# Kernel optimization log

Hardware: AMD Instinct MI355X
Metric: run time of the kernel (lower is better)

Reference implementation:

```python
import jax, jax.numpy as jnp
import numpy as np

N_NODES = 50000
N_EDGES = 800000
FIN = 128
FQK = 128
FV = 128
H = 8


def setup_inputs() -> dict:
    key = jax.random.key(0)
    k1, k2, k3, k4, k5 = jax.random.split(key, 5)
    x = jax.random.normal(k1, (N_NODES, FIN), dtype=jnp.float32)
    # nn.Linear(Fin, 2*Fqk+Fv, bias=False): weight shape [Ftot, Fin]
    W = jax.random.normal(k2, (2 * FQK + FV, FIN), dtype=jnp.float32) / np.sqrt(FIN)
    # src must be sorted (scatter_* assume batch[-1]+1 segments)
    src = jnp.sort(jax.random.randint(k3, (N_EDGES,), 0, N_NODES))
    dest = jax.random.randint(k4, (N_EDGES,), 0, N_NODES)
    ei = jnp.stack([src, dest])
    batch = jnp.sort(jax.random.randint(k5, (N_NODES,), 0, 64))
    return {"x": x, "W": W, "batch": batch, "ei": ei}


def reference(x, W, batch, ei):
    n = x.shape[0]
    Fh = FQK // H    # 16
    Fhv = FV // H    # 16
    scaling = float(Fh) ** (-0.5)
    src, dest = ei[0], ei[1]

    qkv = x @ W.T                                   # [n, 2*Fqk+Fv]
    q = (qkv[:, :FQK] * scaling).reshape(n, H, Fh)
    k = qkv[:, FQK:2 * FQK].reshape(n, H, Fh)
    v = qkv[:, 2 * FQK:].reshape(n, H, Fhv)

    # per-edge attention scores, one per head: [E, H]
    aw = jnp.einsum('ehf,ehf->eh', q[src], k[dest])
    # faithful to original scatter_softmax: subtract GLOBAL per-head max
    aw = aw - aw.max(axis=0)
    ex = jnp.exp(aw)
    denom = jax.ops.segment_sum(ex, src, num_segments=n)[src]   # [E, H]
    a = ex / denom

    out = jax.ops.segment_sum(a[:, :, None] * v[dest], src, num_segments=n)  # [n, H, Fhv]
    return out.reshape(n, H * Fhv)
```

## Files before the change

kernel.cpp:

```cpp
#include <hip/hip_runtime.h>
#include <hip/hip_fp16.h>
#include <math.h>

#define FIN_ 128
#define NGB_ 3

typedef _Float16 half2v __attribute__((ext_vector_type(2)));
typedef _Float16 half8v __attribute__((ext_vector_type(8)));
typedef __attribute__((ext_vector_type(4))) float float4v;

__device__ __forceinline__ half2v u2h(unsigned u) {
    union { unsigned u; half2v h; } c; c.u = u; return c.h;
}

__device__ __forceinline__ half8v cvt8(float4 a, float4 b) {
    half8v r;
    r[0] = (_Float16)a.x; r[1] = (_Float16)a.y;
    r[2] = (_Float16)a.z; r[3] = (_Float16)a.w;
    r[4] = (_Float16)b.x; r[5] = (_Float16)b.y;
    r[6] = (_Float16)b.z; r[7] = (_Float16)b.w;
    return r;
}

__global__ __launch_bounds__(256) void prep_kernel(const float* __restrict__ x,
                                                   const float* __restrict__ W,
                                                   _Float16* __restrict__ qb,
                                                   _Float16* __restrict__ kv,
                                                   const int* __restrict__ src,
                                                   int* __restrict__ rowptr,
                                                   int n, int nE, int nxb) {
    const int bid = blockIdx.x;
    const int t = threadIdx.x;

    if (bid >= 3 * nxb) {
        const int i = (bid - 3 * nxb) * 256 + t;
        if (i > n) return;
        int lo = 0, hi = nE;
        while (lo < hi) {
            int mid = (lo + hi) >> 1;
            if (src[mid] < i) lo = mid + 1; else hi = mid;
        }
        rowptr[i] = lo;
        return;
    }

    __shared__ _Float16 T[64][136];
    const int bx = bid / 3, fsel = bid % 3;
    const int row0 = bx * 128;
    const int f0 = fsel * 128;
    const int lane = t & 63;
    const int wave = t >> 6;
    const int wr = wave >> 1, wc = wave & 1;
    const int l15 = lane & 15, kg = lane >> 4;

    float4v acc[4][4];
#pragma unroll
    for (int i = 0; i < 4; ++i)
#pragma unroll
        for (int j = 0; j < 4; ++j) acc[i][j] = (float4v)0.f;

    int nodeIdx[4];
#pragma unroll
    for (int ni = 0; ni < 4; ++ni) {
        const int nd = row0 + wc * 64 + ni * 16 + l15;
        nodeIdx[ni] = (nd < n) ? nd : 0;
    }
    const size_t fbase = (size_t)(f0 + wr * 64 + l15) * FIN_;

#pragma unroll
    for (int half = 0; half < 2; ++half) {
#pragma unroll
        for (int ks = 0; ks < 2; ++ks) {
            const int koff = half * 64 + ks * 32 + kg * 8;
            half8v a[4], b[4];
#pragma unroll
            for (int mi = 0; mi < 4; ++mi) {
                const float* p = W + fbase + (size_t)mi * 16 * FIN_ + koff;
                a[mi] = cvt8(*(const float4*)p, *(const float4*)(p + 4));
            }
#pragma unroll
            for (int ni = 0; ni < 4; ++ni) {
                const float* p = x + (size_t)nodeIdx[ni] * FIN_ + koff;
                b[ni] = cvt8(*(const float4*)p, *(const float4*)(p + 4));
            }
#pragma unroll
            for (int mi = 0; mi < 4; ++mi)
#pragma unroll
                for (int ni = 0; ni < 4; ++ni)
                    acc[mi][ni] = __builtin_amdgcn_mfma_f32_16x16x32_f16(
                        a[mi], b[ni], acc[mi][ni], 0, 0, 0);
        }
    }

    const bool isq = (fsel == 0);
    const float s = isq ? 0.25f : 1.0f;
    for (int ph = 0; ph < 2; ++ph) {
        if (wc == ph) {
#pragma unroll
            for (int mi = 0; mi < 4; ++mi) {
                const int fb = wr * 64 + mi * 16 + kg * 4;
#pragma unroll
                for (int ni = 0; ni < 4; ++ni) {
                    const int nl = ni * 16 + l15;
                    union { ushort4 u; _Float16 f[4]; } pk;
#pragma unroll
                    for (int r = 0; r < 4; ++r) pk.f[r] = (_Float16)(acc[mi][ni][r] * s);
                    *(ushort4*)&T[nl][fb] = pk.u;
                }
            }
        }
        __syncthreads();
#pragma unroll
        for (int i = 0; i < 4; ++i) {
            const int u = t + i * 256;
            const int nl = u >> 4;
            const int cs = (u & 15) * 8;
            const int ng = row0 + ph * 64 + nl;
            if (ng < n) {
                const half8v val = *(const half8v*)&T[nl][cs];
                if (isq) *(half8v*)&qb[(size_t)ng * 128 + cs] = val;
                else     *(half8v*)&kv[(size_t)ng * 256 + (f0 - 128) + cs] = val;
            }
        }
        __syncthreads();
    }
}

__device__ __forceinline__ float dot16(uint4 k0, uint4 k1, const half2v* q) {
#if __has_builtin(__builtin_amdgcn_fdot2)
    float s = __builtin_amdgcn_fdot2(u2h(k0.x), q[0], 0.f, false);
    s = __builtin_amdgcn_fdot2(u2h(k0.y), q[1], s, false);
    s = __builtin_amdgcn_fdot2(u2h(k0.z), q[2], s, false);
    s = __builtin_amdgcn_fdot2(u2h(k0.w), q[3], s, false);
    s = __builtin_amdgcn_fdot2(u2h(k1.x), q[4], s, false);
    s = __builtin_amdgcn_fdot2(u2h(k1.y), q[5], s, false);
    s = __builtin_amdgcn_fdot2(u2h(k1.z), q[6], s, false);
    s = __builtin_amdgcn_fdot2(u2h(k1.w), q[7], s, false);
    return s;
#else
    half2v a = u2h(k0.x) * q[0];
    a += u2h(k0.y) * q[1];
    a += u2h(k0.z) * q[2];
    a += u2h(k0.w) * q[3];
    a += u2h(k1.x) * q[4];
    a += u2h(k1.y) * q[5];
    a += u2h(k1.z) * q[6];
    a += u2h(k1.w) * q[7];
    return (float)a[0] + (float)a[1];
#endif
}

__global__ __launch_bounds__(256) void attn_edges_ep(const _Float16* __restrict__ qb,
                                                     const _Float16* __restrict__ kv,
                                                     const int* __restrict__ rowptr,
                                                     const int* __restrict__ dest,
                                                     float* __restrict__ out, int n) {
    const int wave = threadIdx.x >> 6;
    const int node = blockIdx.x * 4 + wave;
    if (node >= n) return;
    const int lane = threadIdx.x & 63;
    const int j = lane >> 3;
    const int h = lane & 7;
    const int ppos = ((j & 1) << 3) | ((j & 2) << 1) | ((j & 4) >> 1);
    float* outp = &out[(size_t)node * FIN_ + h * 16 + ppos];

    const int e0 = rowptr[node];
    const int e1 = rowptr[node + 1];
    if (e0 == e1) {
        *(float2*)outp = make_float2(0.f, 0.f);
        return;
    }

    half2v qh[8];
    {
        const uint4 q0 = *(const uint4*)(qb + (size_t)node * 128 + h * 16);
        const uint4 q1 = *(const uint4*)(qb + (size_t)node * 128 + h * 16 + 8);
        qh[0] = u2h(q0.x); qh[1] = u2h(q0.y); qh[2] = u2h(q0.z); qh[3] = u2h(q0.w);
        qh[4] = u2h(q1.x); qh[5] = u2h(q1.y); qh[6] = u2h(q1.z); qh[7] = u2h(q1.w);
    }

    float lsum = 0.f;
    half2v a8[8];
#pragma unroll
    for (int i = 0; i < 8; ++i) a8[i] = (half2v)(_Float16)0;

    const int hoff = h << 4;
    for (int eb = e0; eb < e1; eb += 16) {
        const int eA = eb + j;
        const int eB = eb + 8 + j;
        const bool vA = eA < e1;
        const bool vB = eB < e1;
        const unsigned dA = (unsigned)dest[vA ? eA : (e1 - 1)];
        const unsigned dB = (unsigned)dest[vB ? eB : (e1 - 1)];
        const unsigned offA = (dA << 8) + hoff;
        const unsigned offB = (dB << 8) + hoff;
        const uint4 k0A = *(const uint4*)(kv + offA);
        const uint4 k1A = *(const uint4*)(kv + offA + 8);
        const uint4 v0A = *(const uint4*)(kv + offA + 128);
        const uint4 v1A = *(const uint4*)(kv + offA + 136);
        const uint4 k0B = *(const uint4*)(kv + offB);
        const uint4 k1B = *(const uint4*)(kv + offB + 8);
        const uint4 v0B = *(const uint4*)(kv + offB + 128);
        const uint4 v1B = *(const uint4*)(kv + offB + 136);

        const float sA = dot16(k0A, k1A, qh);
        const float sB = dot16(k0B, k1B, qh);
        const float pA = vA ? __expf(sA) : 0.f;
        const float pB = vB ? __expf(sB) : 0.f;
        lsum += pA + pB;

        const _Float16 ha = (_Float16)pA, hb = (_Float16)pB;
        const half2v pa = {ha, ha}, pb = {hb, hb};
        a8[0] += pa * u2h(v0A.x) + pb * u2h(v0B.x);
        a8[1] += pa * u2h(v0A.y) + pb * u2h(v0B.y);
        a8[2] += pa * u2h(v0A.z) + pb * u2h(v0B.z);
        a8[3] += pa * u2h(v0A.w) + pb * u2h(v0B.w);
        a8[4] += pa * u2h(v1A.x) + pb * u2h(v1B.x);
        a8[5] += pa * u2h(v1A.y) + pb * u2h(v1B.y);
        a8[6] += pa * u2h(v1A.z) + pb * u2h(v1B.z);
        a8[7] += pa * u2h(v1A.w) + pb * u2h(v1B.w);
    }

    lsum += __shfl_xor(lsum, 8);
    lsum += __shfl_xor(lsum, 16);
    lsum += __shfl_xor(lsum, 32);

    float a16[16];
#pragma unroll
    for (int i = 0; i < 8; ++i) {
        a16[2 * i]     = (float)a8[i][0];
        a16[2 * i + 1] = (float)a8[i][1];
    }

    float r8[8];
    {
        const bool b = (j & 1) != 0;
#pragma unroll
        for (int i = 0; i < 8; ++i) {
            const float keep = b ? a16[i + 8] : a16[i];
            const float send = b ? a16[i] : a16[i + 8];
            r8[i] = keep + __shfl_xor(send, 8);
        }
    }
    float r4[4];
    {
        const bool b = (j & 2) != 0;
#pragma unroll
        for (int i = 0; i < 4; ++i) {
            const float keep = b ? r8[i + 4] : r8[i];
            const float send = b ? r8[i] : r8[i + 4];
            r4[i] = keep + __shfl_xor(send, 16);
        }
    }
    float r2[2];
    {
        const bool b = (j & 4) != 0;
#pragma unroll
        for (int i = 0; i < 2; ++i) {
            const float keep = b ? r4[i + 2] : r4[i];
            const float send = b ? r4[i] : r4[i + 2];
            r2[i] = keep + __shfl_xor(send, 32);
        }
    }

    const float inv = (lsum > 0.f) ? 1.f / lsum : 0.f;
    *(float2*)outp = make_float2(r2[0] * inv, r2[1] * inv);
}

extern "C" void kernel_launch(void* const* d_in, const int* in_sizes, int n_in,
                              void* d_out, int out_size, void* d_ws, size_t ws_size,
                              hipStream_t stream) {
    const float* x = (const float*)d_in[0];
    const float* W = (const float*)d_in[1];
    const int* ei = (const int*)d_in[3];

    const int n = in_sizes[0] / FIN_;
    const int nE = in_sizes[3] / 2;
    const int* src = ei;
    const int* dest = ei + nE;

    char* w = (char*)d_ws;
    _Float16* qb = (_Float16*)w;   w += (size_t)n * 128 * 2;
    _Float16* kv = (_Float16*)w;   w += (size_t)n * 256 * 2;
    int* rowptr = (int*)w;
    float* out = (float*)d_out;

    const int nxb = (n + 127) / 128;
    const int nrb = (n + 1 + 255) / 256;
    prep_kernel<<<3 * nxb + nrb, 256, 0, stream>>>(x, W, qb, kv, src, rowptr, n, nE, nxb);

    attn_edges_ep<<<(n + 3) / 4, 256, 0, stream>>>(qb, kv, rowptr, dest, out, n);
}
```

Measured before the change: 104.9 us.

## Retile QKV projection to 32-node blocks computing all 384 features per block

The GEMM part of the prep kernel now gives each block 32 nodes and all three Q/K/V feature groups, in place of 128 nodes by one 128-feature group. Each x row is therefore read once rather than three times, and there are many more, smaller blocks, which improves occupancy and load balance on a GPU with many compute units. The rowptr binary-search blocks move to the front of the grid so they get scheduled early. The trade-off is that W is re-read by every block, though at 384x128 it should stay in cache, and the MFMA tile per wave is smaller, with 12 accumulators per wave rather than 16.

```diff
diff --git a/kernel.cpp b/kernel.cpp
--- a/kernel.cpp
+++ b/kernel.cpp
@@ -3,7 +3,6 @@
 #include <math.h>
 
 #define FIN_ 128
-#define NGB_ 3
 
 typedef _Float16 half2v __attribute__((ext_vector_type(2)));
 typedef _Float16 half8v __attribute__((ext_vector_type(8)));
@@ -28,12 +27,12 @@
                                                    _Float16* __restrict__ kv,
                                                    const int* __restrict__ src,
                                                    int* __restrict__ rowptr,
-                                                   int n, int nE, int nxb) {
+                                                   int n, int nE, int nrb) {
     const int bid = blockIdx.x;
     const int t = threadIdx.x;
 
-    if (bid >= 3 * nxb) {
-        const int i = (bid - 3 * nxb) * 256 + t;
+    if (bid < nrb) {
+        const int i = bid * 256 + t;
         if (i > n) return;
         int lo = 0, hi = nE;
         while (lo < hi) {
@@ -44,82 +43,71 @@
         return;
     }
 
-    __shared__ _Float16 T[64][136];
-    const int bx = bid / 3, fsel = bid % 3;
-    const int row0 = bx * 128;
-    const int f0 = fsel * 128;
+    __shared__ _Float16 T[32][136];
+    const int row0 = (bid - nrb) * 32;
     const int lane = t & 63;
-    const int wave = t >> 6;
-    const int wr = wave >> 1, wc = wave & 1;
+    const int wv = t >> 6;
     const int l15 = lane & 15, kg = lane >> 4;
 
-    float4v acc[4][4];
-#pragma unroll
-    for (int i = 0; i < 4; ++i)
-#pragma unroll
-        for (int j = 0; j < 4; ++j) acc[i][j] = (float4v)0.f;
-
-    int nodeIdx[4];
-#pragma unroll
-    for (int ni = 0; ni < 4; ++ni) {
-        const int nd = row0 + wc * 64 + ni * 16 + l15;
+    float4v acc[6][2];
+#pragma unroll
+    for (int g = 0; g < 6; ++g)
+#pragma unroll
+        for (int j = 0; j < 2; ++j) acc[g][j] = (float4v)0.f;
+
+    int nodeIdx[2];
+#pragma unroll
+    for (int ni = 0; ni < 2; ++ni) {
+        const int nd = row0 + ni * 16 + l15;
         nodeIdx[ni] = (nd < n) ? nd : 0;
     }
-    const size_t fbase = (size_t)(f0 + wr * 64 + l15) * FIN_;
-
-#pragma unroll
-    for (int half = 0; half < 2; ++half) {
-#pragma unroll
-        for (int ks = 0; ks < 2; ++ks) {
-            const int koff = half * 64 + ks * 32 + kg * 8;
-            half8v a[4], b[4];
-#pragma unroll
-            for (int mi = 0; mi < 4; ++mi) {
-                const float* p = W + fbase + (size_t)mi * 16 * FIN_ + koff;
-                a[mi] = cvt8(*(const float4*)p, *(const float4*)(p + 4));
+
+#pragma unroll
+    for (int ks = 0; ks < 4; ++ks) {
+        const int koff = ks * 32 + kg * 8;
+        half8v b[2];
+#pragma unroll
+        for (int ni = 0; ni < 2; ++ni) {
+            const float* p = x + (size_t)nodeIdx[ni] * FIN_ + koff;
+            b[ni] = cvt8(*(const float4*)p, *(const float4*)(p + 4));
+        }
+#pragma unroll
+        for (int g = 0; g < 6; ++g) {
+            const int feat = (wv + 4 * g) * 16 + l15;
+            const float* p = W + (size_t)feat * FIN_ + koff;
+            const half8v a = cvt8(*(const float4*)p, *(const float4*)(p + 4));
+            acc[g][0] = __builtin_amdgcn_mfma_f32_16x16x32_f16(a, b[0], acc[g][0], 0, 0, 0);
+            acc[g][1] = __builtin_amdgcn_mfma_f32_16x16x32_f16(a, b[1], acc[g][1], 0, 0, 0);
+        }
+    }
+
+    for (int ph = 0; ph < 3; ++ph) {
+        const float s = (ph == 0) ? 0.25f : 1.0f;
+#pragma unroll
+        for (int g2 = 0; g2 < 2; ++g2) {
+            const int g = 2 * ph + g2;
+            const int fb = (wv + 4 * g2) * 16 + kg * 4;
+#pragma unroll
+            for (int ni = 0; ni < 2; ++ni) {
+                const int nl = ni * 16 + l15;
+                union { ushort4 u; _Float16 f[4]; } pk;
+#pragma unroll
+                for (int r = 0; r < 4; ++r) pk.f[r] = (_Float16)(acc[g][ni][r] * s);
+                *(ushort4*)&T[nl][fb] = pk.u;
             }
-#pragma unroll
-            for (int ni = 0; ni < 4; ++ni) {
-                const float* p = x + (size_t)nodeIdx[ni] * FIN_ + koff;
-                b[ni] = cvt8(*(const float4*)p, *(const float4*)(p + 4));
-            }
-#pragma unroll
-            for (int mi = 0; mi < 4; ++mi)
-#pragma unroll
-                for (int ni = 0; ni < 4; ++ni)
-                    acc[mi][ni] = __builtin_amdgcn_mfma_f32_16x16x32_f16(
-                        a[mi], b[ni], acc[mi][ni], 0, 0, 0);
-        }
-    }
-
-    const bool isq = (fsel == 0);
-    const float s = isq ? 0.25f : 1.0f;
-    for (int ph = 0; ph < 2; ++ph) {
-        if (wc == ph) {
-#pragma unroll
-            for (int mi = 0; mi < 4; ++mi) {
-                const int fb = wr * 64 + mi * 16 + kg * 4;
-#pragma unroll
-                for (int ni = 0; ni < 4; ++ni) {
-                    const int nl = ni * 16 + l15;
-                    union { ushort4 u; _Float16 f[4]; } pk;
-#pragma unroll
-                    for (int r = 0; r < 4; ++r) pk.f[r] = (_Float16)(acc[mi][ni][r] * s);
-                    *(ushort4*)&T[nl][fb] = pk.u;
-                }
-            }
         }
         __syncthreads();
 #pragma unroll
-        for (int i = 0; i < 4; ++i) {
+        for (int i = 0; i < 2; ++i) {
             const int u = t + i * 256;
             const int nl = u >> 4;
             const int cs = (u & 15) * 8;
-            const int ng = row0 + ph * 64 + nl;
+            const int ng = row0 + nl;
             if (ng < n) {
                 const half8v val = *(const half8v*)&T[nl][cs];
-                if (isq) *(half8v*)&qb[(size_t)ng * 128 + cs] = val;
-                else     *(half8v*)&kv[(size_t)ng * 256 + (f0 - 128) + cs] = val;
+                if (ph == 0)      *(half8v*)&qb[(size_t)ng * 128 + cs] = val;
+                else if (ph == 1) *(half8v*)&kv[(size_t)ng * 256 + cs] = val;
+                else              *(half8v*)&kv[(size_t)ng * 256 + 128 + cs] = val;
             }
         }
         __syncthreads();
@@ -285,9 +273,9 @@
     int* rowptr = (int*)w;
     float* out = (float*)d_out;
 
-    const int nxb = (n + 127) / 128;
     const int nrb = (n + 1 + 255) / 256;
-    prep_kernel<<<3 * nxb + nrb, 256, 0, stream>>>(x, W, qb, kv, src, rowptr, n, nE, nxb);
+    const int ngb = (n + 31) / 32;
+    prep_kernel<<<nrb + ngb, 256, 0, stream>>>(x, W, qb, kv, src, rowptr, n, nE, nrb);
 
     attn_edges_ep<<<(n + 3) / 4, 256, 0, stream>>>(qb, kv, rowptr, dest, out, n);
 }
```

After: 113.9 us. +8.6%, slower.
